# Kernel tuning notes

Hardware: AMD Instinct MI355X
Metric: run time of the kernel (lower is better)

## Reference

```python
import jax, jax.numpy as jnp
import numpy as np

N_NODES = 170000
N_EDGES = 1200000
IN, HID, OUT = 128, 128, 64


def setup_inputs() -> dict:
    key = jax.random.key(0)
    ks = jax.random.split(key, 9)
    feat = jax.random.normal(ks[0], (N_NODES, IN), dtype=jnp.float32)
    src = jax.random.randint(ks[1], (N_EDGES,), 0, N_NODES, dtype=jnp.int32)
    dst = jax.random.randint(ks[2], (N_EDGES,), 0, N_NODES, dtype=jnp.int32)
    # Glorot-uniform style init for the GraphConv weights, zero bias (DGL default)
    def glorot(k, fan_in, fan_out):
        lim = np.sqrt(6.0 / (fan_in + fan_out)).astype(np.float32)
        return jax.random.uniform(k, (fan_in, fan_out), jnp.float32, -lim, lim)
    W0 = glorot(ks[3], IN, HID)
    W1 = glorot(ks[4], HID, HID)
    W2 = glorot(ks[5], HID, OUT)
    b0 = jnp.zeros((HID,), jnp.float32)
    b1 = jnp.zeros((HID,), jnp.float32)
    b2 = jnp.zeros((OUT,), jnp.float32)
    return {"feat": feat, "src": src, "dst": dst,
            "W0": W0, "b0": b0, "W1": W1, "b1": b1, "W2": W2, "b2": b2}


def _gcn_layer(h, src, dst, norm_out, norm_in, W, b, relu):
    # norm='both': D_out^{-1/2} scaling, sum-aggregate over edges, D_in^{-1/2} scaling
    h = h * norm_out                                   # [N, d]
    agg = jax.ops.segment_sum(h[src], dst, num_segments=N_NODES)  # gather+scatter-add
    r = (agg * norm_in) @ W + b                        # dense transform + bias
    return jax.nn.relu(r) if relu else r


def reference(feat, src, dst, W0, b0, W1, b1, W2, b2):
    ones = jnp.ones((N_EDGES,), jnp.float32)
    # DGL clamps degrees to min 1 (allow_zero_in_degree=True keeps zero-degree nodes)
    deg_out = jnp.clip(jax.ops.segment_sum(ones, src, num_segments=N_NODES), 1.0)
    deg_in = jnp.clip(jax.ops.segment_sum(ones, dst, num_segments=N_NODES), 1.0)
    norm_out = (deg_out ** -0.5)[:, None]
    norm_in = (deg_in ** -0.5)[:, None]
    # Dropout(0.5) between layers is identity in eval mode
    h = _gcn_layer(feat, src, dst, norm_out, norm_in, W0, b0, relu=True)
    h = _gcn_layer(h, src, dst, norm_out, norm_in, W1, b1, relu=True)
    h = _gcn_layer(h, src, dst, norm_out, norm_in, W2, b2, relu=False)
    return h
```

## Files before the change

### kernel.cpp

```cpp
#include <hip/hip_runtime.h>
#include <hip/hip_bf16.h>

#define N_NODES 170000
#define N_EDGES 1200000

#define AITEMS 2048
#define NB_A   586
#define NCB    333
#define SCAN_A_N      (NCB * NB_A)
#define SCAN_A_BLOCKS 191
#define SCAN_A_PAD    (SCAN_A_BLOCKS * 1024)
#define HISTA_PAD     195140

#define DOUT_NPC    16384
#define DOUT_WPC    8192
#define DOUT_NCHUNK 11
#define DOUT_NSLICE 96
#define DOUT_SLICE_E (N_EDGES / DOUT_NSLICE)
#define WORDS_N     85000

typedef short bf16x8 __attribute__((ext_vector_type(8)));
typedef float f32x4 __attribute__((ext_vector_type(4)));

__device__ __forceinline__ void bf_split(float v, __hip_bfloat16& h, __hip_bfloat16& l)
{
    h = __float2bfloat16(v);
    l = __float2bfloat16(v - __bfloat162float(h));
}


__global__ __launch_bounds__(256) void coarse_hist_kernel(
    const int* __restrict__ dst, int* __restrict__ histA, int nedges)
{
    __shared__ int h[NCB];
    int t = threadIdx.x;
    for (int j = t; j < NCB; j += 256) h[j] = 0;
    __syncthreads();
    int base = blockIdx.x * AITEMS;
    #pragma unroll
    for (int j = 0; j < AITEMS / 256; j++) {
        int i = base + j * 256 + t;
        if (i < nedges) atomicAdd(&h[dst[i] >> 9], 1);
    }
    __syncthreads();
    for (int j = t; j < NCB; j += 256)
        histA[j * NB_A + blockIdx.x] = h[j];
}

__global__ __launch_bounds__(256) void scan1_kernel(
    const int* __restrict__ in, int* __restrict__ partial,
    int* __restrict__ blockSums, int n)
{
    __shared__ int sdata[256];
    int t = threadIdx.x;
    int base = blockIdx.x * 1024 + t * 4;
    int4 v = make_int4(0, 0, 0, 0);
    if (base + 3 < n) v = *(const int4*)&in[base];
    else {
        if (base + 0 < n) v.x = in[base + 0];
        if (base + 1 < n) v.y = in[base + 1];
        if (base + 2 < n) v.z = in[base + 2];
        if (base + 3 < n) v.w = in[base + 3];
    }
    int tsum = v.x + v.y + v.z + v.w;
    sdata[t] = tsum;
    __syncthreads();
    for (int off = 1; off < 256; off <<= 1) {
        int add = 0;
        if (t >= off) add = sdata[t - off];
        __syncthreads();
        if (t >= off) sdata[t] += add;
        __syncthreads();
    }
    int excl = sdata[t] - tsum;
    int4 o;
    o.x = excl;
    o.y = o.x + v.x;
    o.z = o.y + v.y;
    o.w = o.z + v.z;
    *(int4*)&partial[base] = o;
    if (t == 255) blockSums[blockIdx.x] = sdata[255];
}

__global__ __launch_bounds__(256) void scan2_kernel(int* __restrict__ blockSums, int nb)
{
    __shared__ int sdata[256];
    int t = threadIdx.x;
    int val = (t < nb) ? blockSums[t] : 0;
    sdata[t] = val;
    __syncthreads();
    for (int off = 1; off < 256; off <<= 1) {
        int add = 0;
        if (t >= off) add = sdata[t - off];
        __syncthreads();
        if (t >= off) sdata[t] += add;
        __syncthreads();
    }
    if (t < nb) blockSums[t] = sdata[t] - val;
}

__global__ __launch_bounds__(256) void scan3_kernel(
    int* __restrict__ buf, const int* __restrict__ blockSums)
{
    int off = blockSums[blockIdx.x];
    int base = blockIdx.x * 1024 + threadIdx.x * 4;
    int4 v = *(const int4*)&buf[base];
    v.x += off; v.y += off; v.z += off; v.w += off;
    *(int4*)&buf[base] = v;
}

__global__ __launch_bounds__(256) void coarse_scatter_kernel(
    const int* __restrict__ src, const int* __restrict__ dst,
    const int* __restrict__ scanA, int* __restrict__ pairs, int nedges)
{
    __shared__ int base[NCB];
    __shared__ int cur[NCB];
    int t = threadIdx.x;
    for (int j = t; j < NCB; j += 256) {
        base[j] = scanA[j * NB_A + blockIdx.x];
        cur[j] = 0;
    }
    __syncthreads();
    int eb = blockIdx.x * AITEMS;
    #pragma unroll
    for (int j = 0; j < AITEMS / 256; j++) {
        int i = eb + j * 256 + t;
        if (i < nedges) {
            int d = dst[i];
            int cb = d >> 9;
            int r = atomicAdd(&cur[cb], 1);
            pairs[base[cb] + r] = (src[i] << 9) | (d & 511);
        }
    }
}

__global__ __launch_bounds__(256) void bucket_sort_kernel(
    const int* __restrict__ pairs, const int* __restrict__ scanA,
    int* __restrict__ csr, int* __restrict__ row_start,
    float* __restrict__ norm_in, int nedges)
{
    __shared__ int hist[512];
    __shared__ int curs[512];
    __shared__ int sdata[256];
    int cb = blockIdx.x;
    int t = threadIdx.x;
    int beg = scanA[cb * NB_A];
    int end = (cb == NCB - 1) ? nedges : scanA[(cb + 1) * NB_A];

    hist[t] = 0; hist[t + 256] = 0;
    __syncthreads();
    for (int j = beg + t; j < end; j += 256)
        atomicAdd(&hist[pairs[j] & 511], 1);
    __syncthreads();

    int a = hist[2 * t], b = hist[2 * t + 1];
    sdata[t] = a + b;
    __syncthreads();
    for (int off = 1; off < 256; off <<= 1) {
        int add = 0;
        if (t >= off) add = sdata[t - off];
        __syncthreads();
        if (t >= off) sdata[t] += add;
        __syncthreads();
    }
    int epair = sdata[t] - (a + b);
    curs[2 * t]     = beg + epair;
    curs[2 * t + 1] = beg + epair + a;
    __syncthreads();

    int nodeBase = cb << 9;
    for (int s = t; s < 512; s += 256) {
        int v = nodeBase + s;
        if (v < N_NODES) {
            row_start[v] = curs[s];
            norm_in[v] = rsqrtf(fmaxf((float)hist[s], 1.0f));
        }
    }
    if (cb == NCB - 1 && t == 0) row_start[N_NODES] = nedges;
    __syncthreads();

    for (int j = beg + t; j < end; j += 256) {
        int p = pairs[j];
        int pos = atomicAdd(&curs[p & 511], 1);
        csr[pos] = p >> 9;
    }
}

__global__ __launch_bounds__(256) void degout_hist_kernel(
    const int* __restrict__ src, unsigned* __restrict__ partial)
{
    __shared__ unsigned h[DOUT_WPC];
    int chunk = blockIdx.x / DOUT_NSLICE;
    int slice = blockIdx.x % DOUT_NSLICE;
    int lo = chunk * DOUT_NPC;
    int t = threadIdx.x;
    #pragma unroll
    for (int j = 0; j < DOUT_WPC / 256; j++) h[j * 256 + t] = 0;
    __syncthreads();
    const int4* sp = (const int4*)(src + slice * DOUT_SLICE_E);
    for (int i = t; i < DOUT_SLICE_E / 4; i += 256) {
        int4 v = sp[i];
        unsigned a = (unsigned)(v.x - lo);
        if (a < DOUT_NPC) atomicAdd(&h[a >> 1], 1u << ((a & 1) * 16));
        a = (unsigned)(v.y - lo);
        if (a < DOUT_NPC) atomicAdd(&h[a >> 1], 1u << ((a & 1) * 16));
        a = (unsigned)(v.z - lo);
        if (a < DOUT_NPC) atomicAdd(&h[a >> 1], 1u << ((a & 1) * 16));
        a = (unsigned)(v.w - lo);
        if (a < DOUT_NPC) atomicAdd(&h[a >> 1], 1u << ((a & 1) * 16));
    }
    __syncthreads();
    int wlo = chunk * DOUT_WPC;
    int nw = min(DOUT_WPC, WORDS_N - wlo);
    for (int j = t; j < nw; j += 256)
        partial[(size_t)slice * WORDS_N + wlo + j] = h[j];
}

__global__ __launch_bounds__(256) void degout_combine_kernel(
    const unsigned* __restrict__ partial, float* __restrict__ norm_out)
{
    int w = blockIdx.x * 256 + threadIdx.x;
    if (w >= WORDS_N) return;
    unsigned slo = 0, shi = 0;
    #pragma unroll
    for (int s = 0; s < DOUT_NSLICE; s++) {
        unsigned x = partial[(size_t)s * WORDS_N + w];
        slo += x & 0xFFFFu;
        shi += x >> 16;
    }
    norm_out[2 * w]     = rsqrtf(fmaxf((float)slo, 1.0f));
    norm_out[2 * w + 1] = rsqrtf(fmaxf((float)shi, 1.0f));
}

__global__ __launch_bounds__(256) void f2bf_kernel(
    const float* __restrict__ in, __hip_bfloat16* __restrict__ outp, int n8)
{
    int i = blockIdx.x * 256 + threadIdx.x;
    if (i >= n8) return;
    float4 a = *(const float4*)&in[(size_t)i * 8];
    float4 b = *(const float4*)&in[(size_t)i * 8 + 4];
    float4 packed;
    __hip_bfloat162* p = (__hip_bfloat162*)&packed;
    p[0].x = __float2bfloat16(a.x); p[0].y = __float2bfloat16(a.y);
    p[1].x = __float2bfloat16(a.z); p[1].y = __float2bfloat16(a.w);
    p[2].x = __float2bfloat16(b.x); p[2].y = __float2bfloat16(b.y);
    p[3].x = __float2bfloat16(b.z); p[3].y = __float2bfloat16(b.w);
    *(float4*)&outp[(size_t)i * 8] = packed;
}

__global__ __launch_bounds__(256) void wsplit_kernel(
    const float* __restrict__ W, int nout,
    __hip_bfloat16* __restrict__ Whi, __hip_bfloat16* __restrict__ Wlo)
{
    int i = blockIdx.x * 256 + threadIdx.x;
    if (i >= 128 * nout) return;
    int k = i / nout, n = i - k * nout;
    float v = W[i];
    __hip_bfloat16 h, l;
    bf_split(v, h, l);
    Whi[n * 128 + k] = h;
    Wlo[n * 128 + k] = l;
}


template<int NT, bool RS>
__global__ __launch_bounds__(256) void gemm_kernel(
    const __hip_bfloat16* __restrict__ A,
    const __hip_bfloat16* __restrict__ Wthi, const __hip_bfloat16* __restrict__ Wtlo,
    const float* __restrict__ rowscale, __hip_bfloat16* __restrict__ outp,
    int nrows)
{
    const int OUTW = NT * 16;
    const int wave = threadIdx.x >> 6;
    const int lane = threadIdx.x & 63;
    const int n = lane & 15;
    const int q = lane >> 4;
    const int r0 = blockIdx.x * 128 + wave * 32;
    if (r0 >= nrows) return;
    const bool t1 = (r0 + 16) < nrows;
    const size_t a0off = (size_t)(r0 + n) * 128 + q * 8;
    const size_t a1off = (size_t)(t1 ? (r0 + 16 + n) : (r0 + n)) * 128 + q * 8;
    const size_t bbase = (size_t)n * 128 + q * 8;

    f32x4 acc0[NT], acc1[NT];
    const f32x4 zero = {0.f, 0.f, 0.f, 0.f};
    #pragma unroll
    for (int ct = 0; ct < NT; ct++) { acc0[ct] = zero; acc1[ct] = zero; }

    #pragma unroll 1
    for (int kc = 0; kc < 4; kc++) {
        bf16x8 ah0 = *(const bf16x8*)(A + a0off + kc * 32);
        bf16x8 ah1 = *(const bf16x8*)(A + a1off + kc * 32);
        #pragma unroll
        for (int ct = 0; ct < NT; ct++) {
            bf16x8 bh = *(const bf16x8*)(Wthi + (size_t)ct * 2048 + bbase + kc * 32);
            bf16x8 bl = *(const bf16x8*)(Wtlo + (size_t)ct * 2048 + bbase + kc * 32);
            acc0[ct] = __builtin_amdgcn_mfma_f32_16x16x32_bf16(ah0, bh, acc0[ct], 0, 0, 0);
            acc0[ct] = __builtin_amdgcn_mfma_f32_16x16x32_bf16(ah0, bl, acc0[ct], 0, 0, 0);
            acc1[ct] = __builtin_amdgcn_mfma_f32_16x16x32_bf16(ah1, bh, acc1[ct], 0, 0, 0);
            acc1[ct] = __builtin_amdgcn_mfma_f32_16x16x32_bf16(ah1, bl, acc1[ct], 0, 0, 0);
        }
    }

    #pragma unroll
    for (int r = 0; r < 4; r++) {
        int grow = r0 + q * 4 + r;
        float rs = RS ? rowscale[grow] : 1.f;
        #pragma unroll
        for (int ct = 0; ct < NT; ct++) {
            float v = acc0[ct][r] * rs;
            outp[(size_t)grow * OUTW + ct * 16 + n] = __float2bfloat16(v);
        }
    }
    if (t1) {
        #pragma unroll
        for (int r = 0; r < 4; r++) {
            int grow = r0 + 16 + q * 4 + r;
            float rs = RS ? rowscale[grow] : 1.f;
            #pragma unroll
            for (int ct = 0; ct < NT; ct++) {
                float v = acc1[ct][r] * rs;
                outp[(size_t)grow * OUTW + ct * 16 + n] = __float2bfloat16(v);
            }
        }
    }
}

__global__ __launch_bounds__(256) void gather128_kernel(
    const __hip_bfloat16* __restrict__ t, const int* __restrict__ csr,
    const int* __restrict__ row_start, const float* __restrict__ norm_in,
    const float* __restrict__ bias, __hip_bfloat16* __restrict__ outp)
{
    int tid = blockIdx.x * 256 + threadIdx.x;
    int row = tid >> 4;
    int l = threadIdx.x & 15;
    int gbase = threadIdx.x & 48;
    if (row >= N_NODES) return;
    int beg = row_start[row];
    int end = row_start[row + 1];
    float acc[8] = {};
    for (int j = beg; j < end; j += 16) {
        int cnt = min(16, end - j);
        int sv = 0;
        float wv = 0.f;
        if (j + l < end) { sv = csr[j + l]; wv = 1.f; }
        int s0 = __shfl(sv, gbase);
        if (j + l >= end) sv = s0;
        #pragma unroll
        for (int ib = 0; ib < 16; ib += 8) {
            if (ib < cnt) {
                float4 rg[8];
                float ww[8];
                #pragma unroll
                for (int k = 0; k < 8; k++) {
                    int s = __shfl(sv, gbase + ib + k);
                    ww[k] = __shfl(wv, gbase + ib + k);
                    rg[k] = *(const float4*)(t + (size_t)s * 128 + l * 8);
                }
                #pragma unroll
                for (int k = 0; k < 8; k++) {
                    const __hip_bfloat162* pp = (const __hip_bfloat162*)&rg[k];
                    float sc = ww[k];
                    float2 f0 = __bfloat1622float2(pp[0]);
                    float2 f1 = __bfloat1622float2(pp[1]);
                    float2 f2 = __bfloat1622float2(pp[2]);
                    float2 f3 = __bfloat1622float2(pp[3]);
                    acc[0] += f0.x * sc; acc[1] += f0.y * sc;
                    acc[2] += f1.x * sc; acc[3] += f1.y * sc;
                    acc[4] += f2.x * sc; acc[5] += f2.y * sc;
                    acc[6] += f3.x * sc; acc[7] += f3.y * sc;
                }
            }
        }
    }
    float ni = norm_in[row];
    float4 b0 = *(const float4*)&bias[l * 8];
    float4 b1 = *(const float4*)&bias[l * 8 + 4];
    float bb[8] = {b0.x, b0.y, b0.z, b0.w, b1.x, b1.y, b1.z, b1.w};
    float4 packed;
    __hip_bfloat16* hp = (__hip_bfloat16*)&packed;
    #pragma unroll
    for (int k = 0; k < 8; k++)
        hp[k] = __float2bfloat16(fmaxf(acc[k] * ni + bb[k], 0.f));
    *(float4*)(outp + (size_t)row * 128 + l * 8) = packed;
}

__global__ __launch_bounds__(256) void final_gather_kernel(
    const __hip_bfloat16* __restrict__ h, const int* __restrict__ csr,
    const int* __restrict__ row_start, const float* __restrict__ norm_in,
    const float* __restrict__ bias, float* __restrict__ outf)
{
    int tid = blockIdx.x * 256 + threadIdx.x;
    int row = tid >> 4;
    int l = threadIdx.x & 15;
    int gbase = threadIdx.x & 48;
    if (row >= N_NODES) return;
    int beg = row_start[row];
    int end = row_start[row + 1];
    float acc[4] = {};
    for (int j = beg; j < end; j += 16) {
        int cnt = min(16, end - j);
        int sv = 0;
        float wv = 0.f;
        if (j + l < end) { sv = csr[j + l]; wv = 1.f; }
        int s0 = __shfl(sv, gbase);
        if (j + l >= end) sv = s0;
        #pragma unroll
        for (int ib = 0; ib < 16; ib += 8) {
            if (ib < cnt) {
                float2 rg[8];
                float ww[8];
                #pragma unroll
                for (int k = 0; k < 8; k++) {
                    int s = __shfl(sv, gbase + ib + k);
                    ww[k] = __shfl(wv, gbase + ib + k);
                    rg[k] = *(const float2*)(h + (size_t)s * 64 + l * 4);
                }
                #pragma unroll
                for (int k = 0; k < 8; k++) {
                    const __hip_bfloat162* pp = (const __hip_bfloat162*)&rg[k];
                    float sc = ww[k];
                    float2 f0 = __bfloat1622float2(pp[0]);
                    float2 f1 = __bfloat1622float2(pp[1]);
                    acc[0] += f0.x * sc; acc[1] += f0.y * sc;
                    acc[2] += f1.x * sc; acc[3] += f1.y * sc;
                }
            }
        }
    }
    float ni = norm_in[row];
    float4 o0 = make_float4(acc[0] * ni, acc[1] * ni, acc[2] * ni, acc[3] * ni);
    float4 b = *(const float4*)&bias[l * 4];
    o0.x += b.x; o0.y += b.y; o0.z += b.z; o0.w += b.w;
    *(float4*)&outf[(size_t)row * 64 + l * 4] = o0;
}

extern "C" void kernel_launch(void* const* d_in, const int* in_sizes, int n_in,
                              void* d_out, int out_size, void* d_ws, size_t ws_size,
                              hipStream_t stream)
{
    const float* feat = (const float*)d_in[0];
    const int* src    = (const int*)d_in[1];
    const int* dst    = (const int*)d_in[2];
    const float* W0   = (const float*)d_in[3];
    const float* b0   = (const float*)d_in[4];
    const float* W1   = (const float*)d_in[5];
    const float* b1   = (const float*)d_in[6];
    const float* W2   = (const float*)d_in[7];
    const float* b2   = (const float*)d_in[8];
    float* out = (float*)d_out;

    const int N = N_NODES;
    const int E = N_EDGES;

    char* ws = (char*)d_ws;
    float* norm_out = (float*)ws;
    float* norm_in  = norm_out + N;
    int* row_start  = (int*)(norm_in + N);
    int* csr        = row_start + 170004;
    __hip_bfloat16* Wt0hi = (__hip_bfloat16*)(csr + E);
    __hip_bfloat16* Wt0lo = Wt0hi + 16384;
    __hip_bfloat16* Wt1hi = Wt0lo + 16384;
    __hip_bfloat16* Wt1lo = Wt1hi + 16384;
    __hip_bfloat16* Wt2hi = Wt1lo + 16384;
    __hip_bfloat16* Wt2lo = Wt2hi + 8192;
    __hip_bfloat16* P0 = Wt2lo + 8192;
    __hip_bfloat16* P1 = P0 + (size_t)N * 128;
    __hip_bfloat16* aux = P1 + (size_t)N * 128;
    int* histA          = (int*)P1;
    int* scanA          = histA + HISTA_PAD;
    int* blockSumsA     = scanA + SCAN_A_PAD + 4;
    unsigned* partial   = (unsigned*)(blockSumsA + 256);
    int* pairs          = (int*)aux;

    degout_hist_kernel<<<DOUT_NCHUNK * DOUT_NSLICE, 256, 0, stream>>>(src, partial);
    degout_combine_kernel<<<(WORDS_N + 255) / 256, 256, 0, stream>>>(partial, norm_out);
    coarse_hist_kernel<<<NB_A, 256, 0, stream>>>(dst, histA, E);
    scan1_kernel<<<SCAN_A_BLOCKS, 256, 0, stream>>>(histA, scanA, blockSumsA, SCAN_A_N);
    scan2_kernel<<<1, 256, 0, stream>>>(blockSumsA, SCAN_A_BLOCKS);
    scan3_kernel<<<SCAN_A_BLOCKS, 256, 0, stream>>>(scanA, blockSumsA);
    coarse_scatter_kernel<<<NB_A, 256, 0, stream>>>(src, dst, scanA, pairs, E);
    bucket_sort_kernel<<<NCB, 256, 0, stream>>>(pairs, scanA, csr, row_start, norm_in, E);
    f2bf_kernel<<<(N * 16 + 255) / 256, 256, 0, stream>>>(feat, P0, N * 16);
    wsplit_kernel<<<64, 256, 0, stream>>>(W0, 128, Wt0hi, Wt0lo);
    wsplit_kernel<<<64, 256, 0, stream>>>(W1, 128, Wt1hi, Wt1lo);
    wsplit_kernel<<<32, 256, 0, stream>>>(W2, 64, Wt2hi, Wt2lo);

    const int mmBlocks = (N + 127) / 128;
    const int gatherBlocks = (N * 16 + 255) / 256;

    gemm_kernel<8, true><<<mmBlocks, 256, 0, stream>>>(P0, Wt0hi, Wt0lo, norm_out, P1, N);
    gather128_kernel<<<gatherBlocks, 256, 0, stream>>>(P1, csr, row_start, norm_in, b0, P0);

    gemm_kernel<8, true><<<mmBlocks, 256, 0, stream>>>(P0, Wt1hi, Wt1lo, norm_out, P1, N);
    gather128_kernel<<<gatherBlocks, 256, 0, stream>>>(P1, csr, row_start, norm_in, b1, P0);

    gemm_kernel<4, true><<<mmBlocks, 256, 0, stream>>>(P0, Wt2hi, Wt2lo, norm_out, P1, N);
    final_gather_kernel<<<gatherBlocks, 256, 0, stream>>>(P1, csr, row_start, norm_in, b2, out);
}
```

Baseline: 573.2 us.

## Fuse gather-aggregate with the next layer's GEMM via LDS tile

```diff
diff --git a/kernel.cpp b/kernel.cpp
--- a/kernel.cpp
+++ b/kernel.cpp
@@ -26,6 +26,11 @@
 {
     h = __float2bfloat16(v);
     l = __float2bfloat16(v - __bfloat162float(h));
+}
+
+__device__ __forceinline__ int lds_addr(int row, int col)
+{
+    return (row * 256 + col * 2) ^ ((row & 7) << 4);
 }
 
 
@@ -262,6 +267,109 @@
     Wlo[n * 128 + k] = l;
 }
 
+template<int NT>
+__global__ __launch_bounds__(64) void fused_gather_gemm_kernel(
+    const __hip_bfloat16* __restrict__ t, const int* __restrict__ csr,
+    const int* __restrict__ row_start, const float* __restrict__ norm_in,
+    const float* __restrict__ bias, const float* __restrict__ rowscale,
+    const __hip_bfloat16* __restrict__ Wthi, const __hip_bfloat16* __restrict__ Wtlo,
+    __hip_bfloat16* __restrict__ outp)
+{
+    __shared__ __align__(16) unsigned char smem[4096];
+    const int rbase = blockIdx.x * 16;
+    const int tx = threadIdx.x;
+    const int l = tx & 15;
+    const int g = tx >> 4;
+    const int gbase = tx & 48;
+
+    for (int rr = 0; rr < 4; rr++) {
+        const int lrow = g * 4 + rr;
+        const int row = rbase + lrow;
+        float acc[8] = {};
+        float ni = 0.f;
+        if (row < N_NODES) {
+            ni = norm_in[row];
+            int beg = row_start[row];
+            int end = row_start[row + 1];
+            for (int j = beg; j < end; j += 16) {
+                int cnt = min(16, end - j);
+                int sv = 0;
+                float wv = 0.f;
+                if (j + l < end) { sv = csr[j + l]; wv = 1.f; }
+                int s0 = __shfl(sv, gbase);
+                if (j + l >= end) sv = s0;
+                #pragma unroll
+                for (int ib = 0; ib < 16; ib += 8) {
+                    if (ib < cnt) {
+                        float4 rg[8];
+                        float ww[8];
+                        #pragma unroll
+                        for (int k = 0; k < 8; k++) {
+                            int s = __shfl(sv, gbase + ib + k);
+                            ww[k] = __shfl(wv, gbase + ib + k);
+                            rg[k] = *(const float4*)(t + (size_t)s * 128 + l * 8);
+                        }
+                        #pragma unroll
+                        for (int k = 0; k < 8; k++) {
+                            const __hip_bfloat162* pp = (const __hip_bfloat162*)&rg[k];
+                            float sc = ww[k];
+                            float2 f0 = __bfloat1622float2(pp[0]);
+                            float2 f1 = __bfloat1622float2(pp[1]);
+                            float2 f2 = __bfloat1622float2(pp[2]);
+                            float2 f3 = __bfloat1622float2(pp[3]);
+                            acc[0] += f0.x * sc; acc[1] += f0.y * sc;
+                            acc[2] += f1.x * sc; acc[3] += f1.y * sc;
+                            acc[4] += f2.x * sc; acc[5] += f2.y * sc;
+                            acc[6] += f3.x * sc; acc[7] += f3.y * sc;
+                        }
+                    }
+                }
+            }
+        }
+        float4 b0 = *(const float4*)&bias[l * 8];
+        float4 b1 = *(const float4*)&bias[l * 8 + 4];
+        float bb[8] = {b0.x, b0.y, b0.z, b0.w, b1.x, b1.y, b1.z, b1.w};
+        float4 packed;
+        __hip_bfloat16* hp = (__hip_bfloat16*)&packed;
+        #pragma unroll
+        for (int k = 0; k < 8; k++)
+            hp[k] = __float2bfloat16(fmaxf(acc[k] * ni + bb[k], 0.f));
+        *(float4*)(smem + lds_addr(lrow, l * 8)) = packed;
+    }
+    __syncthreads();
+
+    const int n = tx & 15;
+    const int q = tx >> 4;
+    const size_t bbase = (size_t)n * 128 + q * 8;
+    const f32x4 zero = {0.f, 0.f, 0.f, 0.f};
+    f32x4 acc[NT];
+    #pragma unroll
+    for (int ct = 0; ct < NT; ct++) acc[ct] = zero;
+
+    #pragma unroll
+    for (int kc = 0; kc < 4; kc++) {
+        bf16x8 a = *(const bf16x8*)(smem + lds_addr(n, q * 8 + kc * 32));
+        #pragma unroll
+        for (int ct = 0; ct < NT; ct++) {
+            bf16x8 bh = *(const bf16x8*)(Wthi + (size_t)ct * 2048 + bbase + kc * 32);
+            bf16x8 bl = *(const bf16x8*)(Wtlo + (size_t)ct * 2048 + bbase + kc * 32);
+            acc[ct] = __builtin_amdgcn_mfma_f32_16x16x32_bf16(a, bh, acc[ct], 0, 0, 0);
+            acc[ct] = __builtin_amdgcn_mfma_f32_16x16x32_bf16(a, bl, acc[ct], 0, 0, 0);
+        }
+    }
+
+    #pragma unroll
+    for (int r = 0; r < 4; r++) {
+        int grow = rbase + q * 4 + r;
+        if (grow < N_NODES) {
+            float rs = rowscale[grow];
+            #pragma unroll
+            for (int ct = 0; ct < NT; ct++)
+                outp[(size_t)grow * (NT * 16) + ct * 16 + n] =
+                    __float2bfloat16(acc[ct][r] * rs);
+        }
+    }
+}
 
 template<int NT, bool RS>
 __global__ __launch_bounds__(256) void gemm_kernel(
@@ -324,65 +432,6 @@
             }
         }
     }
-}
-
-__global__ __launch_bounds__(256) void gather128_kernel(
-    const __hip_bfloat16* __restrict__ t, const int* __restrict__ csr,
-    const int* __restrict__ row_start, const float* __restrict__ norm_in,
-    const float* __restrict__ bias, __hip_bfloat16* __restrict__ outp)
-{
-    int tid = blockIdx.x * 256 + threadIdx.x;
-    int row = tid >> 4;
-    int l = threadIdx.x & 15;
-    int gbase = threadIdx.x & 48;
-    if (row >= N_NODES) return;
-    int beg = row_start[row];
-    int end = row_start[row + 1];
-    float acc[8] = {};
-    for (int j = beg; j < end; j += 16) {
-        int cnt = min(16, end - j);
-        int sv = 0;
-        float wv = 0.f;
-        if (j + l < end) { sv = csr[j + l]; wv = 1.f; }
-        int s0 = __shfl(sv, gbase);
-        if (j + l >= end) sv = s0;
-        #pragma unroll
-        for (int ib = 0; ib < 16; ib += 8) {
-            if (ib < cnt) {
-                float4 rg[8];
-                float ww[8];
-                #pragma unroll
-                for (int k = 0; k < 8; k++) {
-                    int s = __shfl(sv, gbase + ib + k);
-                    ww[k] = __shfl(wv, gbase + ib + k);
-                    rg[k] = *(const float4*)(t + (size_t)s * 128 + l * 8);
-                }
-                #pragma unroll
-                for (int k = 0; k < 8; k++) {
-                    const __hip_bfloat162* pp = (const __hip_bfloat162*)&rg[k];
-                    float sc = ww[k];
-                    float2 f0 = __bfloat1622float2(pp[0]);
-                    float2 f1 = __bfloat1622float2(pp[1]);
-                    float2 f2 = __bfloat1622float2(pp[2]);
-                    float2 f3 = __bfloat1622float2(pp[3]);
-                    acc[0] += f0.x * sc; acc[1] += f0.y * sc;
-                    acc[2] += f1.x * sc; acc[3] += f1.y * sc;
-                    acc[4] += f2.x * sc; acc[5] += f2.y * sc;
-                    acc[6] += f3.x * sc; acc[7] += f3.y * sc;
-                }
-            }
-        }
-    }
-    float ni = norm_in[row];
-    float4 b0 = *(const float4*)&bias[l * 8];
-    float4 b1 = *(const float4*)&bias[l * 8 + 4];
-    float bb[8] = {b0.x, b0.y, b0.z, b0.w, b1.x, b1.y, b1.z, b1.w};
-    float4 packed;
-    __hip_bfloat16* hp = (__hip_bfloat16*)&packed;
-    #pragma unroll
-    for (int k = 0; k < 8; k++)
-        hp[k] = __float2bfloat16(fmaxf(acc[k] * ni + bb[k], 0.f));
-    *(float4*)(outp + (size_t)row * 128 + l * 8) = packed;
 }
 
 __global__ __launch_bounds__(256) void final_gather_kernel(
@@ -487,14 +536,17 @@
     wsplit_kernel<<<32, 256, 0, stream>>>(W2, 64, Wt2hi, Wt2lo);
 
     const int mmBlocks = (N + 127) / 128;
+    const int fggBlocks = (N + 15) / 16;
     const int gatherBlocks = (N * 16 + 255) / 256;
 
     gemm_kernel<8, true><<<mmBlocks, 256, 0, stream>>>(P0, Wt0hi, Wt0lo, norm_out, P1, N);
-    gather128_kernel<<<gatherBlocks, 256, 0, stream>>>(P1, csr, row_start, norm_in, b0, P0);
-
-    gemm_kernel<8, true><<<mmBlocks, 256, 0, stream>>>(P0, Wt1hi, Wt1lo, norm_out, P1, N);
-    gather128_kernel<<<gatherBlocks, 256, 0, stream>>>(P1, csr, row_start, norm_in, b1, P0);
-
-    gemm_kernel<4, true><<<mmBlocks, 256, 0, stream>>>(P0, Wt2hi, Wt2lo, norm_out, P1, N);
-    final_gather_kernel<<<gatherBlocks, 256, 0, stream>>>(P1, csr, row_start, norm_in, b2, out);
-}
+
+    fused_gather_gemm_kernel<8><<<fggBlocks, 64, 0, stream>>>(
+        P1, csr, row_start, norm_in, b0, norm_out, Wt1hi, Wt1lo, P0);
+
+    fused_gather_gemm_kernel<4><<<fggBlocks, 64, 0, stream>>>(
+        P0, csr, row_start, norm_in, b1, norm_out, Wt2hi, Wt2lo, P1);
+
+    final_gather_kernel<<<gatherBlocks, 256, 0, stream>>>(
+        P1, csr, row_start, norm_in, b2, out);
+}
```

New measurement: 591.1 us. 1.03x slower.

## Stage GEMM A tile into LDS via async global_load_lds with XOR swizzle

Applied to the files above, without the earlier changes.

```diff
diff --git a/kernel.cpp b/kernel.cpp
--- a/kernel.cpp
+++ b/kernel.cpp
@@ -26,6 +26,13 @@
 {
     h = __float2bfloat16(v);
     l = __float2bfloat16(v - __bfloat162float(h));
+}
+
+__device__ __forceinline__ void async_copy16(const void* g, void* l)
+{
+    __builtin_amdgcn_global_load_lds(
+        (const __attribute__((address_space(1))) void*)g,
+        (__attribute__((address_space(3))) void*)l, 16, 0, 0);
 }
 
 
@@ -248,20 +255,28 @@
     *(float4*)&outp[(size_t)i * 8] = packed;
 }
 
-__global__ __launch_bounds__(256) void wsplit_kernel(
-    const float* __restrict__ W, int nout,
-    __hip_bfloat16* __restrict__ Whi, __hip_bfloat16* __restrict__ Wlo)
+__global__ __launch_bounds__(256) void wsplit_all_kernel(
+    const float* __restrict__ W0, const float* __restrict__ W1,
+    const float* __restrict__ W2,
+    __hip_bfloat16* __restrict__ Wt0hi, __hip_bfloat16* __restrict__ Wt0lo,
+    __hip_bfloat16* __restrict__ Wt1hi, __hip_bfloat16* __restrict__ Wt1lo,
+    __hip_bfloat16* __restrict__ Wt2hi, __hip_bfloat16* __restrict__ Wt2lo)
 {
     int i = blockIdx.x * 256 + threadIdx.x;
-    if (i >= 128 * nout) return;
-    int k = i / nout, n = i - k * nout;
-    float v = W[i];
+    const float* W;
+    __hip_bfloat16 *Whi, *Wlo;
+    int nout, j;
+    if (i < 16384)      { W = W0; Whi = Wt0hi; Wlo = Wt0lo; nout = 128; j = i; }
+    else if (i < 32768) { W = W1; Whi = Wt1hi; Wlo = Wt1lo; nout = 128; j = i - 16384; }
+    else if (i < 40960) { W = W2; Whi = Wt2hi; Wlo = Wt2lo; nout = 64;  j = i - 32768; }
+    else return;
+    int k = j / nout, nn = j - k * nout;
+    float v = W[j];
     __hip_bfloat16 h, l;
     bf_split(v, h, l);
-    Whi[n * 128 + k] = h;
-    Wlo[n * 128 + k] = l;
-}
-
+    Whi[nn * 128 + k] = h;
+    Wlo[nn * 128 + k] = l;
+}
 
 template<int NT, bool RS>
 __global__ __launch_bounds__(256) void gemm_kernel(
@@ -271,15 +286,29 @@
     int nrows)
 {
     const int OUTW = NT * 16;
-    const int wave = threadIdx.x >> 6;
-    const int lane = threadIdx.x & 63;
-    const int n = lane & 15;
-    const int q = lane >> 4;
-    const int r0 = blockIdx.x * 128 + wave * 32;
+    __shared__ __align__(16) unsigned char smem[32768];
+    const int wv = threadIdx.x >> 6;
+    const int ln = threadIdx.x & 63;
+    const int vr = min(128, nrows - blockIdx.x * 128);
+    const char* Ab = (const char*)A + (size_t)blockIdx.x * 128 * 256;
+
+    #pragma unroll
+    for (int j = 0; j < 8; j++) {
+        int slot = j * 4096 + wv * 1024 + ln * 16;
+        int row = slot >> 8;
+        int srcoff = slot ^ ((row & 7) << 4);
+        if (row >= vr) srcoff &= 255;
+        async_copy16(Ab + srcoff, smem + j * 4096 + wv * 1024);
+    }
+    __syncthreads();
+
+    const int n = ln & 15;
+    const int q = ln >> 4;
+    const int r0 = blockIdx.x * 128 + wv * 32;
     if (r0 >= nrows) return;
     const bool t1 = (r0 + 16) < nrows;
-    const size_t a0off = (size_t)(r0 + n) * 128 + q * 8;
-    const size_t a1off = (size_t)(t1 ? (r0 + 16 + n) : (r0 + n)) * 128 + q * 8;
+    const int lr0 = wv * 32 + n;
+    const int lr1 = t1 ? (lr0 + 16) : lr0;
     const size_t bbase = (size_t)n * 128 + q * 8;
 
     f32x4 acc0[NT], acc1[NT];
@@ -289,8 +318,11 @@
 
     #pragma unroll 1
     for (int kc = 0; kc < 4; kc++) {
-        bf16x8 ah0 = *(const bf16x8*)(A + a0off + kc * 32);
-        bf16x8 ah1 = *(const bf16x8*)(A + a1off + kc * 32);
+        int bc = (q * 8 + kc * 32) * 2;
+        int c0 = (lr0 * 256 + bc) ^ ((lr0 & 7) << 4);
+        int c1 = (lr1 * 256 + bc) ^ ((lr1 & 7) << 4);
+        bf16x8 ah0 = *(const bf16x8*)(smem + c0);
+        bf16x8 ah1 = *(const bf16x8*)(smem + c1);
         #pragma unroll
         for (int ct = 0; ct < NT; ct++) {
             bf16x8 bh = *(const bf16x8*)(Wthi + (size_t)ct * 2048 + bbase + kc * 32);
@@ -472,6 +504,7 @@
     int* blockSumsA     = scanA + SCAN_A_PAD + 4;
     unsigned* partial   = (unsigned*)(blockSumsA + 256);
     int* pairs          = (int*)aux;
+    __hip_bfloat16* featbf = aux;
 
     degout_hist_kernel<<<DOUT_NCHUNK * DOUT_NSLICE, 256, 0, stream>>>(src, partial);
     degout_combine_kernel<<<(WORDS_N + 255) / 256, 256, 0, stream>>>(partial, norm_out);
@@ -481,20 +514,22 @@
     scan3_kernel<<<SCAN_A_BLOCKS, 256, 0, stream>>>(scanA, blockSumsA);
     coarse_scatter_kernel<<<NB_A, 256, 0, stream>>>(src, dst, scanA, pairs, E);
     bucket_sort_kernel<<<NCB, 256, 0, stream>>>(pairs, scanA, csr, row_start, norm_in, E);
-    f2bf_kernel<<<(N * 16 + 255) / 256, 256, 0, stream>>>(feat, P0, N * 16);
-    wsplit_kernel<<<64, 256, 0, stream>>>(W0, 128, Wt0hi, Wt0lo);
-    wsplit_kernel<<<64, 256, 0, stream>>>(W1, 128, Wt1hi, Wt1lo);
-    wsplit_kernel<<<32, 256, 0, stream>>>(W2, 64, Wt2hi, Wt2lo);
+    f2bf_kernel<<<(N * 16 + 255) / 256, 256, 0, stream>>>(feat, featbf, N * 16);
+    wsplit_all_kernel<<<160, 256, 0, stream>>>(W0, W1, W2, Wt0hi, Wt0lo,
+                                               Wt1hi, Wt1lo, Wt2hi, Wt2lo);
 
     const int mmBlocks = (N + 127) / 128;
     const int gatherBlocks = (N * 16 + 255) / 256;
 
-    gemm_kernel<8, true><<<mmBlocks, 256, 0, stream>>>(P0, Wt0hi, Wt0lo, norm_out, P1, N);
+    gemm_kernel<8, true><<<mmBlocks, 256, 0, stream>>>(
+        featbf, Wt0hi, Wt0lo, norm_out, P1, N);
     gather128_kernel<<<gatherBlocks, 256, 0, stream>>>(P1, csr, row_start, norm_in, b0, P0);
 
-    gemm_kernel<8, true><<<mmBlocks, 256, 0, stream>>>(P0, Wt1hi, Wt1lo, norm_out, P1, N);
+    gemm_kernel<8, true><<<mmBlocks, 256, 0, stream>>>(
+        P0, Wt1hi, Wt1lo, norm_out, P1, N);
     gather128_kernel<<<gatherBlocks, 256, 0, stream>>>(P1, csr, row_start, norm_in, b1, P0);
 
-    gemm_kernel<4, true><<<mmBlocks, 256, 0, stream>>>(P0, Wt2hi, Wt2lo, norm_out, P1, N);
+    gemm_kernel<4, true><<<mmBlocks, 256, 0, stream>>>(
+        P0, Wt2hi, Wt2lo, norm_out, P1, N);
     final_gather_kernel<<<gatherBlocks, 256, 0, stream>>>(P1, csr, row_start, norm_in, b2, out);
 }
```

Result: faster. 559.7 us (-2.3%).
